# Performance work log

Hardware: AMD Instinct MI355X
Metric: run time of the kernel (lower is better)

Reference implementation:

```python
import jax, jax.numpy as jnp
import numpy as np

H, W, BS, CIN = 224, 608, 1, 128
CLS = (16, 12, 10)
PAD = (0, 2, 3)
C12 = CLS[0] * CLS[1]            # 192
C123 = C12 * CLS[2]              # 1920
SUPER = 384
CFACT = C123 // SUPER            # 5
PAD_PROJ = 0.1


def _p(key, shape):
    return jax.random.normal(key, shape, dtype=jnp.float32) * 0.05


def setup_inputs() -> dict:
    key = jax.random.key(0)
    ks = iter(jax.random.split(key, 32))
    d = {"x_in": jax.random.normal(next(ks), (BS, CIN, H, W), dtype=jnp.float32)}
    # stage-1: grouped 1x1 convs (groups=height -> one [out,in] matmul per image line)
    for i, (ci, co) in enumerate([(32, 32), (32, 32), (32, CLS[0] + 2 * PAD[0])]):
        d[f"w1_{i}"] = _p(next(ks), (H, co, ci))
        d[f"b1_{i}"] = _p(next(ks), (H, co))
    # stage-2: CondMul tables indexed by line*16 + stage-1 class
    for i, (ci, co) in enumerate([(32, 32), (32, 32), (32, CLS[1] + 2 * PAD[1])]):
        d[f"w2_{i}"] = _p(next(ks), (H * CLS[0], ci, co))
        d[f"b2_{i}"] = _p(next(ks), (H * CLS[0], co))
    # stage-3: CondMul tables indexed by line*192 + stage-12 class
    for i, (ci, co) in enumerate([(32, 32), (32, 32), (32, CLS[2] + 2 * PAD[2])]):
        d[f"w3_{i}"] = _p(next(ks), (H * C12, ci, co))
        d[f"b3_{i}"] = _p(next(ks), (H * C12, co))
    d["wr0"] = _p(next(ks), (H * SUPER, 32, 32))
    d["br0"] = _p(next(ks), (H * SUPER, 32))
    d["wr1"] = _p(next(ks), (H * C123, 32, 1))
    d["br1"] = _p(next(ks), (H * C123, 1))
    return d


def _condmul(x, inds, w, b):
    # CondMul: y[n] = x[n] @ w[inds[n]] + b[inds[n]]
    return jnp.einsum('ni,nio->no', x, w[inds]) + b[inds]


def _forward(x_in, w1, b1, w2, b2, w3, b3, wr0, br0, wr1, br1):
    bs, _, h, w_ = x_in.shape
    lrelu = jax.nn.leaky_relu  # negative_slope=0.01, same as torch default
    offsets = jnp.arange(h, dtype=jnp.int32).reshape(1, 1, h, 1)
    # ---- stage 1: per-line 1x1 grouped conv stack -> argmax class
    x = x_in[:, 0:32].transpose(0, 2, 1, 3)                    # [b,h,32,w]
    for i in range(3):
        x = jnp.einsum('bhiw,hoi->bhow', x, w1[i]) + b1[i][None, :, :, None]
        if i < 2:
            x = lrelu(x)
    x = x.transpose(0, 2, 1, 3)                                 # [b,16,h,w]
    inds1 = jnp.argmax(x, axis=1)[:, None].astype(jnp.int32)    # [b,1,h,w]
    inds1_l = (inds1 + CLS[0] * offsets).reshape(-1)
    # ---- stage 2: CondMul chain conditioned on (line, class1)
    x = x_in[:, 32:64].transpose(0, 2, 3, 1).reshape(-1, 32)    # [N,32]
    for i in range(3):
        x = _condmul(x, inds1_l, w2[i], b2[i])
        if i < 2:
            x = lrelu(x)
    inds2 = jnp.argmax(x, axis=1).astype(jnp.int32).reshape(bs, 1, h, w_)
    inds12 = inds1 * CLS[1] + (inds2 - PAD[1])
    inds12_l = (jnp.clip(inds12, 0, C12 - 1) + C12 * offsets).reshape(-1)
    # ---- stage 3: CondMul chain conditioned on (line, class12)
    x = x_in[:, 64:96].transpose(0, 2, 3, 1).reshape(-1, 32)
    for i in range(3):
        if i < 2:
            x = lrelu(_condmul(x, inds12_l, w3[i], b3[i]))
        else:
            x = _condmul(x, inds12_l, w3[i], b3[i])
    inds3 = jnp.argmax(x, axis=1).astype(jnp.int32).reshape(bs, 1, h, w_)
    inds123 = jnp.clip(inds12 * CLS[2] + (inds3 - PAD[2]), 0, C123 - 1)
    inds = inds123.reshape(-1)
    lines = jnp.broadcast_to(offsets, (bs, 1, h, w_)).reshape(-1)
    inds_l = inds + C123 * lines                                 # per-leaf index
    inds_super_l = inds // CFACT + SUPER * lines                 # superclass index (reg_line_div=1)
    x = x_in[:, 96:128].transpose(0, 2, 3, 1).reshape(-1, 32)
    x = lrelu(_condmul(x, inds_super_l, wr0, br0))
    r = _condmul(x, inds_l, wr1, br1)[:, 0]                      # [N]
    out = (inds.astype(jnp.float32) + r).reshape(bs, 1, h, w_) / float(C123)
    out = (out - PAD_PROJ) / (1.0 - 2.0 * PAD_PROJ)              # undo projector padding
    return out


def reference(x_in, w1_0, b1_0, w1_1, b1_1, w1_2, b1_2,
              w2_0, b2_0, w2_1, b2_1, w2_2, b2_2,
              w3_0, b3_0, w3_1, b3_1, w3_2, b3_2,
              wr0, br0, wr1, br1):
    return _forward(x_in,
                    (w1_0, w1_1, w1_2), (b1_0, b1_1, b1_2),
                    (w2_0, w2_1, w2_2), (b2_0, b2_1, b2_2),
                    (w3_0, w3_1, w3_2), (b3_0, b3_1, b3_2),
                    wr0, br0, wr1, br1)
```

## Files before the change

### kernel.cpp

```cpp
#include <hip/hip_runtime.h>
#include <cstddef>

#define HH 224
#define WW 608
#define HWSZ (HH * WW)

__device__ __forceinline__ float lrelu(float v) { return v > 0.0f ? v : 0.01f * v; }

template <int CO>
__device__ __forceinline__ void cm4(const float* __restrict__ wmat,
                                    const float* __restrict__ bvec,
                                    int s, const float (&act)[8], float (&acc)[CO / 4]) {
    constexpr int CH = CO / 4;
#pragma unroll
    for (int j = 0; j < CH; j++) acc[j] = 0.0f;
#pragma unroll
    for (int sp = 0; sp < 4; sp++) {
#pragma unroll
        for (int ii = 0; ii < 8; ii++) {
            float xi = __shfl(act[ii], sp, 4);
            const float* wr = wmat + (sp * 8 + ii) * CO + s * CH;
            if constexpr (CH == 8) {
                float4 a = *reinterpret_cast<const float4*>(wr);
                float4 b = *reinterpret_cast<const float4*>(wr + 4);
                acc[0] = fmaf(xi, a.x, acc[0]); acc[1] = fmaf(xi, a.y, acc[1]);
                acc[2] = fmaf(xi, a.z, acc[2]); acc[3] = fmaf(xi, a.w, acc[3]);
                acc[4] = fmaf(xi, b.x, acc[4]); acc[5] = fmaf(xi, b.y, acc[5]);
                acc[6] = fmaf(xi, b.z, acc[6]); acc[7] = fmaf(xi, b.w, acc[7]);
            } else {
                float4 a = *reinterpret_cast<const float4*>(wr);
                acc[0] = fmaf(xi, a.x, acc[0]); acc[1] = fmaf(xi, a.y, acc[1]);
                acc[2] = fmaf(xi, a.z, acc[2]); acc[3] = fmaf(xi, a.w, acc[3]);
            }
        }
    }
#pragma unroll
    for (int j = 0; j < CH; j++) acc[j] += bvec[s * CH + j];
}

__device__ __forceinline__ void wb_lrelu8(float (&act)[8], const float (&acc)[8]) {
#pragma unroll
    for (int j = 0; j < 8; j++) act[j] = lrelu(acc[j]);
}

__device__ __forceinline__ int argmax4(const float (&v)[4], int s) {
    float bv = v[0];
    int bi = 4 * s;
#pragma unroll
    for (int j = 1; j < 4; j++) {
        if (v[j] > bv) { bv = v[j]; bi = 4 * s + j; }
    }
#pragma unroll
    for (int m = 1; m <= 2; m <<= 1) {
        float ov = __shfl_xor(bv, m, 4);
        int oi = __shfl_xor(bi, m, 4);
        if (ov > bv || (ov == bv && oi < bi)) { bv = ov; bi = oi; }
    }
    return bi;
}

extern "C" __global__ __launch_bounds__(256, 4)
void regressor_fused(const float* __restrict__ x_in,
                     const float* __restrict__ w1_0, const float* __restrict__ b1_0,
                     const float* __restrict__ w1_1, const float* __restrict__ b1_1,
                     const float* __restrict__ w1_2, const float* __restrict__ b1_2,
                     const float* __restrict__ w2_0, const float* __restrict__ b2_0,
                     const float* __restrict__ w2_1, const float* __restrict__ b2_1,
                     const float* __restrict__ w2_2, const float* __restrict__ b2_2,
                     const float* __restrict__ w3_0, const float* __restrict__ b3_0,
                     const float* __restrict__ w3_1, const float* __restrict__ b3_1,
                     const float* __restrict__ w3_2, const float* __restrict__ b3_2,
                     const float* __restrict__ wr0, const float* __restrict__ br0,
                     const float* __restrict__ wr1, const float* __restrict__ br1,
                     float* __restrict__ out) {
    const int bid = blockIdx.x;
    const int r = bid & 7;
    const int t = bid >> 3;
    const int xblk = t % 10;
    const int g = t / 10;
    const int h = 8 * g + r;

    const int tid = threadIdx.x;
    const int p = tid >> 2;
    const int s = tid & 3;
    const int w = xblk * 64 + p;
    const bool valid = (w < WW);
    const int wc = valid ? w : (WW - 1);
    const int base = h * WW + wc;

    __shared__ __align__(16) float sW0[1024];
    __shared__ __align__(16) float sW1[1024];
    __shared__ __align__(16) float sW2[512];
    for (int tt = tid; tt < 1024; tt += 256) {
        int i = tt >> 5, o = tt & 31;
        sW0[tt] = w1_0[h * 1024 + o * 32 + i];
        sW1[tt] = w1_1[h * 1024 + o * 32 + i];
    }
    for (int tt = tid; tt < 512; tt += 256) {
        int i = tt >> 4, o = tt & 15;
        sW2[tt] = w1_2[h * 512 + o * 32 + i];
    }
    __syncthreads();

    float act1[8], act2[8], act3[8], actr[8], acc8[8], acc4[4];

#pragma unroll
    for (int ii = 0; ii < 8; ii++) {
        act1[ii] = x_in[(8 * s + ii) * HWSZ + base];
        act2[ii] = x_in[(32 + 8 * s + ii) * HWSZ + base];
        act3[ii] = x_in[(64 + 8 * s + ii) * HWSZ + base];
        actr[ii] = x_in[(96 + 8 * s + ii) * HWSZ + base];
    }

    cm4<32>(sW0, b1_0 + h * 32, s, act1, acc8);
    wb_lrelu8(act1, acc8);
    cm4<32>(sW1, b1_1 + h * 32, s, act1, acc8);
    wb_lrelu8(act1, acc8);
    cm4<16>(sW2, b1_2 + h * 16, s, act1, acc4);
    const int i1 = argmax4(acc4, s);

    const size_t idx2 = (size_t)h * 16 + (size_t)i1;
    cm4<32>(w2_0 + idx2 * 1024, b2_0 + idx2 * 32, s, act2, acc8);
    wb_lrelu8(act2, acc8);
    cm4<32>(w2_1 + idx2 * 1024, b2_1 + idx2 * 32, s, act2, acc8);
    wb_lrelu8(act2, acc8);
    cm4<16>(w2_2 + idx2 * 512, b2_2 + idx2 * 16, s, act2, acc4);
    const int i2 = argmax4(acc4, s);

    const int inds12 = i1 * 12 + (i2 - 2);
    const int c12 = min(max(inds12, 0), 191);
    const size_t idx3 = (size_t)h * 192 + (size_t)c12;

    cm4<32>(w3_0 + idx3 * 1024, b3_0 + idx3 * 32, s, act3, acc8);
    wb_lrelu8(act3, acc8);
    cm4<32>(w3_1 + idx3 * 1024, b3_1 + idx3 * 32, s, act3, acc8);
    wb_lrelu8(act3, acc8);
    cm4<16>(w3_2 + idx3 * 512, b3_2 + idx3 * 16, s, act3, acc4);
    const int i3 = argmax4(acc4, s);

    const int inds123 = min(max(inds12 * 10 + (i3 - 3), 0), 1919);

    const size_t idxs = (size_t)h * 384 + (size_t)(inds123 / 5);
    cm4<32>(wr0 + idxs * 1024, br0 + idxs * 32, s, actr, acc8);
    wb_lrelu8(actr, acc8);

    const size_t idxr = (size_t)h * 1920 + (size_t)inds123;
    const float* __restrict__ wr1r = wr1 + idxr * 32 + 8 * s;
    float4 wa = *reinterpret_cast<const float4*>(wr1r);
    float4 wb = *reinterpret_cast<const float4*>(wr1r + 4);
    float rpart = 0.0f;
    rpart = fmaf(actr[0], wa.x, rpart); rpart = fmaf(actr[1], wa.y, rpart);
    rpart = fmaf(actr[2], wa.z, rpart); rpart = fmaf(actr[3], wa.w, rpart);
    rpart = fmaf(actr[4], wb.x, rpart); rpart = fmaf(actr[5], wb.y, rpart);
    rpart = fmaf(actr[6], wb.z, rpart); rpart = fmaf(actr[7], wb.w, rpart);
    rpart += __shfl_xor(rpart, 1, 4);
    rpart += __shfl_xor(rpart, 2, 4);
    const float rr = rpart + br1[idxr];

    if (s == 0 && valid) {
        float v = ((float)inds123 + rr) * (1.0f / 1920.0f);
        out[h * WW + w] = (v - 0.1f) * 1.25f;
    }
}

extern "C" void kernel_launch(void* const* d_in, const int* in_sizes, int n_in,
                              void* d_out, int out_size, void* d_ws, size_t ws_size,
                              hipStream_t stream) {
    const float* p[23];
    for (int i = 0; i < 23; i++) p[i] = (const float*)d_in[i];
    regressor_fused<<<dim3(2240), 256, 0, stream>>>(
        p[0],
        p[1], p[2], p[3], p[4], p[5], p[6],
        p[7], p[8], p[9], p[10], p[11], p[12],
        p[13], p[14], p[15], p[16], p[17], p[18],
        p[19], p[20], p[21], p[22],
        (float*)d_out);
}
```

Measured before the change: 137.7 us.

## Process two pixels per thread group to reuse weights and raise ILP

Each 4-thread group now evaluates two pixels (64 apart) through the whole classifier/regressor chain, interleaving their dot products in a dual CondMul helper. The grid is halved, so the per-line stage-1 weight staging into shared memory is amortized over twice the pixels. Input activations are loaded per stage rather than all up front, trading register lifetime for more in-flight independent work. This raises register pressure and reduces block count, which could limit occupancy or cause spills.

```diff
diff --git a/kernel.cpp b/kernel.cpp
--- a/kernel.cpp
+++ b/kernel.cpp
@@ -8,34 +8,47 @@
 __device__ __forceinline__ float lrelu(float v) { return v > 0.0f ? v : 0.01f * v; }
 
 template <int CO>
-__device__ __forceinline__ void cm4(const float* __restrict__ wmat,
-                                    const float* __restrict__ bvec,
-                                    int s, const float (&act)[8], float (&acc)[CO / 4]) {
+__device__ __forceinline__ void cm4_dual(const float* __restrict__ wA, const float* __restrict__ bA,
+                                         const float* __restrict__ wB, const float* __restrict__ bB,
+                                         int s,
+                                         const float (&actA)[8], const float (&actB)[8],
+                                         float (&accA)[CO / 4], float (&accB)[CO / 4]) {
     constexpr int CH = CO / 4;
 #pragma unroll
-    for (int j = 0; j < CH; j++) acc[j] = 0.0f;
+    for (int j = 0; j < CH; j++) { accA[j] = 0.0f; accB[j] = 0.0f; }
 #pragma unroll
     for (int sp = 0; sp < 4; sp++) {
 #pragma unroll
         for (int ii = 0; ii < 8; ii++) {
-            float xi = __shfl(act[ii], sp, 4);
-            const float* wr = wmat + (sp * 8 + ii) * CO + s * CH;
+            float xa = __shfl(actA[ii], sp, 4);
+            float xb = __shfl(actB[ii], sp, 4);
+            const float* ra = wA + (sp * 8 + ii) * CO + s * CH;
+            const float* rb = wB + (sp * 8 + ii) * CO + s * CH;
             if constexpr (CH == 8) {
-                float4 a = *reinterpret_cast<const float4*>(wr);
-                float4 b = *reinterpret_cast<const float4*>(wr + 4);
-                acc[0] = fmaf(xi, a.x, acc[0]); acc[1] = fmaf(xi, a.y, acc[1]);
-                acc[2] = fmaf(xi, a.z, acc[2]); acc[3] = fmaf(xi, a.w, acc[3]);
-                acc[4] = fmaf(xi, b.x, acc[4]); acc[5] = fmaf(xi, b.y, acc[5]);
-                acc[6] = fmaf(xi, b.z, acc[6]); acc[7] = fmaf(xi, b.w, acc[7]);
+                float4 a0 = *reinterpret_cast<const float4*>(ra);
+                float4 a1 = *reinterpret_cast<const float4*>(ra + 4);
+                float4 b0 = *reinterpret_cast<const float4*>(rb);
+                float4 b1 = *reinterpret_cast<const float4*>(rb + 4);
+                accA[0] = fmaf(xa, a0.x, accA[0]); accA[1] = fmaf(xa, a0.y, accA[1]);
+                accA[2] = fmaf(xa, a0.z, accA[2]); accA[3] = fmaf(xa, a0.w, accA[3]);
+                accA[4] = fmaf(xa, a1.x, accA[4]); accA[5] = fmaf(xa, a1.y, accA[5]);
+                accA[6] = fmaf(xa, a1.z, accA[6]); accA[7] = fmaf(xa, a1.w, accA[7]);
+                accB[0] = fmaf(xb, b0.x, accB[0]); accB[1] = fmaf(xb, b0.y, accB[1]);
+                accB[2] = fmaf(xb, b0.z, accB[2]); accB[3] = fmaf(xb, b0.w, accB[3]);
+                accB[4] = fmaf(xb, b1.x, accB[4]); accB[5] = fmaf(xb, b1.y, accB[5]);
+                accB[6] = fmaf(xb, b1.z, accB[6]); accB[7] = fmaf(xb, b1.w, accB[7]);
             } else {
-                float4 a = *reinterpret_cast<const float4*>(wr);
-                acc[0] = fmaf(xi, a.x, acc[0]); acc[1] = fmaf(xi, a.y, acc[1]);
-                acc[2] = fmaf(xi, a.z, acc[2]); acc[3] = fmaf(xi, a.w, acc[3]);
+                float4 a0 = *reinterpret_cast<const float4*>(ra);
+                float4 b0 = *reinterpret_cast<const float4*>(rb);
+                accA[0] = fmaf(xa, a0.x, accA[0]); accA[1] = fmaf(xa, a0.y, accA[1]);
+                accA[2] = fmaf(xa, a0.z, accA[2]); accA[3] = fmaf(xa, a0.w, accA[3]);
+                accB[0] = fmaf(xb, b0.x, accB[0]); accB[1] = fmaf(xb, b0.y, accB[1]);
+                accB[2] = fmaf(xb, b0.z, accB[2]); accB[3] = fmaf(xb, b0.w, accB[3]);
             }
         }
     }
 #pragma unroll
-    for (int j = 0; j < CH; j++) acc[j] += bvec[s * CH + j];
+    for (int j = 0; j < CH; j++) { accA[j] += bA[s * CH + j]; accB[j] += bB[s * CH + j]; }
 }
 
 __device__ __forceinline__ void wb_lrelu8(float (&act)[8], const float (&acc)[8]) {
@@ -76,17 +89,19 @@
     const int bid = blockIdx.x;
     const int r = bid & 7;
     const int t = bid >> 3;
-    const int xblk = t % 10;
-    const int g = t / 10;
+    const int xblk = t % 5;
+    const int g = t / 5;
     const int h = 8 * g + r;
 
     const int tid = threadIdx.x;
-    const int p = tid >> 2;
+    const int slot = tid >> 2;
     const int s = tid & 3;
-    const int w = xblk * 64 + p;
-    const bool valid = (w < WW);
-    const int wc = valid ? w : (WW - 1);
-    const int base = h * WW + wc;
+    const int wA = xblk * 128 + slot;
+    const int wB = xblk * 128 + 64 + slot;
+    const bool validB = (wB < WW);
+    const int wBc = validB ? wB : (WW - 1);
+    const int baseA = h * WW + wA;
+    const int baseB = h * WW + wBc;
 
     __shared__ __align__(16) float sW0[1024];
     __shared__ __align__(16) float sW1[1024];
@@ -102,64 +117,105 @@
     }
     __syncthreads();
 
-    float act1[8], act2[8], act3[8], actr[8], acc8[8], acc4[4];
-
-#pragma unroll
-    for (int ii = 0; ii < 8; ii++) {
-        act1[ii] = x_in[(8 * s + ii) * HWSZ + base];
-        act2[ii] = x_in[(32 + 8 * s + ii) * HWSZ + base];
-        act3[ii] = x_in[(64 + 8 * s + ii) * HWSZ + base];
-        actr[ii] = x_in[(96 + 8 * s + ii) * HWSZ + base];
-    }
-
-    cm4<32>(sW0, b1_0 + h * 32, s, act1, acc8);
-    wb_lrelu8(act1, acc8);
-    cm4<32>(sW1, b1_1 + h * 32, s, act1, acc8);
-    wb_lrelu8(act1, acc8);
-    cm4<16>(sW2, b1_2 + h * 16, s, act1, acc4);
-    const int i1 = argmax4(acc4, s);
-
-    const size_t idx2 = (size_t)h * 16 + (size_t)i1;
-    cm4<32>(w2_0 + idx2 * 1024, b2_0 + idx2 * 32, s, act2, acc8);
-    wb_lrelu8(act2, acc8);
-    cm4<32>(w2_1 + idx2 * 1024, b2_1 + idx2 * 32, s, act2, acc8);
-    wb_lrelu8(act2, acc8);
-    cm4<16>(w2_2 + idx2 * 512, b2_2 + idx2 * 16, s, act2, acc4);
-    const int i2 = argmax4(acc4, s);
-
-    const int inds12 = i1 * 12 + (i2 - 2);
-    const int c12 = min(max(inds12, 0), 191);
-    const size_t idx3 = (size_t)h * 192 + (size_t)c12;
-
-    cm4<32>(w3_0 + idx3 * 1024, b3_0 + idx3 * 32, s, act3, acc8);
-    wb_lrelu8(act3, acc8);
-    cm4<32>(w3_1 + idx3 * 1024, b3_1 + idx3 * 32, s, act3, acc8);
-    wb_lrelu8(act3, acc8);
-    cm4<16>(w3_2 + idx3 * 512, b3_2 + idx3 * 16, s, act3, acc4);
-    const int i3 = argmax4(acc4, s);
-
-    const int inds123 = min(max(inds12 * 10 + (i3 - 3), 0), 1919);
-
-    const size_t idxs = (size_t)h * 384 + (size_t)(inds123 / 5);
-    cm4<32>(wr0 + idxs * 1024, br0 + idxs * 32, s, actr, acc8);
-    wb_lrelu8(actr, acc8);
-
-    const size_t idxr = (size_t)h * 1920 + (size_t)inds123;
-    const float* __restrict__ wr1r = wr1 + idxr * 32 + 8 * s;
-    float4 wa = *reinterpret_cast<const float4*>(wr1r);
-    float4 wb = *reinterpret_cast<const float4*>(wr1r + 4);
-    float rpart = 0.0f;
-    rpart = fmaf(actr[0], wa.x, rpart); rpart = fmaf(actr[1], wa.y, rpart);
-    rpart = fmaf(actr[2], wa.z, rpart); rpart = fmaf(actr[3], wa.w, rpart);
-    rpart = fmaf(actr[4], wb.x, rpart); rpart = fmaf(actr[5], wb.y, rpart);
-    rpart = fmaf(actr[6], wb.z, rpart); rpart = fmaf(actr[7], wb.w, rpart);
-    rpart += __shfl_xor(rpart, 1, 4);
-    rpart += __shfl_xor(rpart, 2, 4);
-    const float rr = rpart + br1[idxr];
-
-    if (s == 0 && valid) {
-        float v = ((float)inds123 + rr) * (1.0f / 1920.0f);
-        out[h * WW + w] = (v - 0.1f) * 1.25f;
+    float actA[8], actB[8], accA[8], accB[8], ac4A[4], ac4B[4];
+
+#pragma unroll
+    for (int ii = 0; ii < 8; ii++) {
+        actA[ii] = x_in[(8 * s + ii) * HWSZ + baseA];
+        actB[ii] = x_in[(8 * s + ii) * HWSZ + baseB];
+    }
+    cm4_dual<32>(sW0, b1_0 + h * 32, sW0, b1_0 + h * 32, s, actA, actB, accA, accB);
+    wb_lrelu8(actA, accA); wb_lrelu8(actB, accB);
+    cm4_dual<32>(sW1, b1_1 + h * 32, sW1, b1_1 + h * 32, s, actA, actB, accA, accB);
+    wb_lrelu8(actA, accA); wb_lrelu8(actB, accB);
+    cm4_dual<16>(sW2, b1_2 + h * 16, sW2, b1_2 + h * 16, s, actA, actB, ac4A, ac4B);
+    const int i1A = argmax4(ac4A, s);
+    const int i1B = argmax4(ac4B, s);
+
+#pragma unroll
+    for (int ii = 0; ii < 8; ii++) {
+        actA[ii] = x_in[(32 + 8 * s + ii) * HWSZ + baseA];
+        actB[ii] = x_in[(32 + 8 * s + ii) * HWSZ + baseB];
+    }
+    const size_t i2A_ = (size_t)h * 16 + (size_t)i1A;
+    const size_t i2B_ = (size_t)h * 16 + (size_t)i1B;
+    cm4_dual<32>(w2_0 + i2A_ * 1024, b2_0 + i2A_ * 32, w2_0 + i2B_ * 1024, b2_0 + i2B_ * 32,
+                 s, actA, actB, accA, accB);
+    wb_lrelu8(actA, accA); wb_lrelu8(actB, accB);
+    cm4_dual<32>(w2_1 + i2A_ * 1024, b2_1 + i2A_ * 32, w2_1 + i2B_ * 1024, b2_1 + i2B_ * 32,
+                 s, actA, actB, accA, accB);
+    wb_lrelu8(actA, accA); wb_lrelu8(actB, accB);
+    cm4_dual<16>(w2_2 + i2A_ * 512, b2_2 + i2A_ * 16, w2_2 + i2B_ * 512, b2_2 + i2B_ * 16,
+                 s, actA, actB, ac4A, ac4B);
+    const int i2A = argmax4(ac4A, s);
+    const int i2B = argmax4(ac4B, s);
+
+    const int inds12A = i1A * 12 + (i2A - 2);
+    const int inds12B = i1B * 12 + (i2B - 2);
+    const size_t i3A_ = (size_t)h * 192 + (size_t)min(max(inds12A, 0), 191);
+    const size_t i3B_ = (size_t)h * 192 + (size_t)min(max(inds12B, 0), 191);
+
+#pragma unroll
+    for (int ii = 0; ii < 8; ii++) {
+        actA[ii] = x_in[(64 + 8 * s + ii) * HWSZ + baseA];
+        actB[ii] = x_in[(64 + 8 * s + ii) * HWSZ + baseB];
+    }
+    cm4_dual<32>(w3_0 + i3A_ * 1024, b3_0 + i3A_ * 32, w3_0 + i3B_ * 1024, b3_0 + i3B_ * 32,
+                 s, actA, actB, accA, accB);
+    wb_lrelu8(actA, accA); wb_lrelu8(actB, accB);
+    cm4_dual<32>(w3_1 + i3A_ * 1024, b3_1 + i3A_ * 32, w3_1 + i3B_ * 1024, b3_1 + i3B_ * 32,
+                 s, actA, actB, accA, accB);
+    wb_lrelu8(actA, accA); wb_lrelu8(actB, accB);
+    cm4_dual<16>(w3_2 + i3A_ * 512, b3_2 + i3A_ * 16, w3_2 + i3B_ * 512, b3_2 + i3B_ * 16,
+                 s, actA, actB, ac4A, ac4B);
+    const int i3A = argmax4(ac4A, s);
+    const int i3B = argmax4(ac4B, s);
+
+    const int leafA = min(max(inds12A * 10 + (i3A - 3), 0), 1919);
+    const int leafB = min(max(inds12B * 10 + (i3B - 3), 0), 1919);
+
+#pragma unroll
+    for (int ii = 0; ii < 8; ii++) {
+        actA[ii] = x_in[(96 + 8 * s + ii) * HWSZ + baseA];
+        actB[ii] = x_in[(96 + 8 * s + ii) * HWSZ + baseB];
+    }
+    const size_t isA = (size_t)h * 384 + (size_t)(leafA / 5);
+    const size_t isB = (size_t)h * 384 + (size_t)(leafB / 5);
+    cm4_dual<32>(wr0 + isA * 1024, br0 + isA * 32, wr0 + isB * 1024, br0 + isB * 32,
+                 s, actA, actB, accA, accB);
+    wb_lrelu8(actA, accA); wb_lrelu8(actB, accB);
+
+    const size_t irA = (size_t)h * 1920 + (size_t)leafA;
+    const size_t irB = (size_t)h * 1920 + (size_t)leafB;
+    const float* ra = wr1 + irA * 32 + 8 * s;
+    const float* rb = wr1 + irB * 32 + 8 * s;
+    float4 wa0 = *reinterpret_cast<const float4*>(ra);
+    float4 wa1 = *reinterpret_cast<const float4*>(ra + 4);
+    float4 wb0 = *reinterpret_cast<const float4*>(rb);
+    float4 wb1 = *reinterpret_cast<const float4*>(rb + 4);
+    float rpA = 0.0f, rpB = 0.0f;
+    rpA = fmaf(actA[0], wa0.x, rpA); rpA = fmaf(actA[1], wa0.y, rpA);
+    rpA = fmaf(actA[2], wa0.z, rpA); rpA = fmaf(actA[3], wa0.w, rpA);
+    rpA = fmaf(actA[4], wa1.x, rpA); rpA = fmaf(actA[5], wa1.y, rpA);
+    rpA = fmaf(actA[6], wa1.z, rpA); rpA = fmaf(actA[7], wa1.w, rpA);
+    rpB = fmaf(actB[0], wb0.x, rpB); rpB = fmaf(actB[1], wb0.y, rpB);
+    rpB = fmaf(actB[2], wb0.z, rpB); rpB = fmaf(actB[3], wb0.w, rpB);
+    rpB = fmaf(actB[4], wb1.x, rpB); rpB = fmaf(actB[5], wb1.y, rpB);
+    rpB = fmaf(actB[6], wb1.z, rpB); rpB = fmaf(actB[7], wb1.w, rpB);
+    rpA += __shfl_xor(rpA, 1, 4);
+    rpA += __shfl_xor(rpA, 2, 4);
+    rpB += __shfl_xor(rpB, 1, 4);
+    rpB += __shfl_xor(rpB, 2, 4);
+    const float rA = rpA + br1[irA];
+    const float rB = rpB + br1[irB];
+
+    if (s == 0) {
+        float vA = ((float)leafA + rA) * (1.0f / 1920.0f);
+        out[baseA] = (vA - 0.1f) * 1.25f;
+        if (validB) {
+            float vB = ((float)leafB + rB) * (1.0f / 1920.0f);
+            out[h * WW + wB] = (vB - 0.1f) * 1.25f;
+        }
     }
 }
 
@@ -168,7 +224,7 @@
                               hipStream_t stream) {
     const float* p[23];
     for (int i = 0; i < 23; i++) p[i] = (const float*)d_in[i];
-    regressor_fused<<<dim3(2240), 256, 0, stream>>>(
+    regressor_fused<<<dim3(1120), 256, 0, stream>>>(
         p[0],
         p[1], p[2], p[3], p[4], p[5], p[6],
         p[7], p[8], p[9], p[10], p[11], p[12],
```

After: 202.6 us. 47.1% more time.
